# Performance work log

Measured on AMD Instinct MI355X. Metric: run time of the kernel, lower is better.

The kernel has to match this reference:

```python
import jax, jax.numpy as jnp
import numpy as np
from jax import lax

B, C, H, W = 32, 512, 14, 14
NA = 9
N = H * W * NA  # 1764 anchors per image
IOU_THR = 0.3
SCORE_THR = 0.5
TOPK = 50


def setup_inputs() -> dict:
    key = jax.random.key(0)
    ks = jax.random.split(key, 8)
    def w(k, shape):
        return jax.random.normal(k, shape, jnp.float32) * 0.01  # nn.init.normal_(std=0.01)
    inp = {"features": jax.random.normal(ks[0], (B, C, H, W), jnp.float32)}
    # bbox head: 512->256 (GN32) ->128 (GN16) ->128 (GN16) -> 4*NA (1x1)
    inp["b1w"] = w(ks[1], (256, 512, 3, 3)); inp["b1b"] = jnp.zeros(256)
    inp["bg1w"] = jnp.ones(256); inp["bg1b"] = jnp.zeros(256)
    inp["b2w"] = w(ks[2], (128, 256, 3, 3)); inp["b2b"] = jnp.zeros(128)
    inp["bg2w"] = jnp.ones(128); inp["bg2b"] = jnp.zeros(128)
    inp["b3w"] = w(ks[3], (128, 128, 3, 3)); inp["b3b"] = jnp.zeros(128)
    inp["bg3w"] = jnp.ones(128); inp["bg3b"] = jnp.zeros(128)
    inp["b4w"] = w(ks[4], (4 * NA, 128, 1, 1)); inp["b4b"] = jnp.zeros(4 * NA)
    # classification head: 512->256 (GN32) ->128 (GN16) -> NA (1x1)
    inp["c1w"] = w(ks[5], (256, 512, 3, 3)); inp["c1b"] = jnp.zeros(256)
    inp["cg1w"] = jnp.ones(256); inp["cg1b"] = jnp.zeros(256)
    inp["c2w"] = w(ks[6], (128, 256, 3, 3)); inp["c2b"] = jnp.zeros(128)
    inp["cg2w"] = jnp.ones(128); inp["cg2b"] = jnp.zeros(128)
    inp["c3w"] = w(ks[7], (NA, 128, 1, 1)); inp["c3b"] = jnp.zeros(NA)
    return inp


def conv(x, w, b):
    k = w.shape[-1]
    pad = ((k // 2, k // 2), (k // 2, k // 2))
    y = lax.conv_general_dilated(x, w, (1, 1), pad, dimension_numbers=("NCHW", "OIHW", "NCHW"))
    return y + b[None, :, None, None]


def group_norm(x, w, b, groups, eps=1e-5):
    Bn, Cn, Hn, Wn = x.shape
    xg = x.reshape(Bn, groups, Cn // groups, Hn, Wn)
    mu = xg.mean(axis=(2, 3, 4), keepdims=True)
    var = xg.var(axis=(2, 3, 4), keepdims=True)
    xg = (xg - mu) * lax.rsqrt(var + eps)
    return xg.reshape(Bn, Cn, Hn, Wn) * w[None, :, None, None] + b[None, :, None, None]


def gelu(x):
    return jax.nn.gelu(x, approximate=False)  # torch nn.GELU default (erf)


def nms_single(boxes, scores):
    # boxes [N,4], scores [N]; greedy NMS, fixed-shape padded output [TOPK,5]
    valid = scores > SCORE_THR
    boxes = jnp.clip(boxes, 0.0, 1.0)
    order = jnp.argsort(-jnp.where(valid, scores, -jnp.inf))  # desc, invalid last
    b = boxes[order]; s = scores[order]; v = valid[order]
    x1 = jnp.maximum(b[:, None, 0], b[None, :, 0])
    y1 = jnp.maximum(b[:, None, 1], b[None, :, 1])
    x2 = jnp.minimum(b[:, None, 2], b[None, :, 2])
    y2 = jnp.minimum(b[:, None, 3], b[None, :, 3])
    inter = jnp.clip(x2 - x1, 0.0) * jnp.clip(y2 - y1, 0.0)
    area = (b[:, 2] - b[:, 0]) * (b[:, 3] - b[:, 1])
    iou = inter / (area[:, None] + area[None, :] - inter)
    # torch keeps when iou < thr; NaN compares False -> suppressed. Replicate exactly:
    suppress = jnp.logical_not(iou < IOU_THR)  # [N,N] bool
    idxs = jnp.arange(N)
    def body(suppressed, xs):
        row, i, vi = xs
        keep_i = vi & jnp.logical_not(suppressed[i])
        return suppressed | (keep_i & row & (idxs > i)), keep_i
    _, keep = lax.scan(body, jnp.zeros(N, bool), (suppress, idxs, v))
    kept_scores = jnp.where(keep, s, -1.0)
    topv, topi = lax.top_k(kept_scores, TOPK)  # first <=50 kept in score order
    out_boxes = jnp.where(topv[:, None] > 0.0, b[topi], 0.0)
    return jnp.concatenate([out_boxes, topv[:, None]], axis=-1)  # [TOPK, 5]; score=-1 marks pad


def _forward(features, b1w, b1b, bg1w, bg1b, b2w, b2b, bg2w, bg2b, b3w, b3b, bg3w, bg3b, b4w, b4b, c1w, c1b, cg1w, cg1b, c2w, c2b, cg2w, cg2b, c3w, c3b):
    bs = features.shape[0]
    h = group_norm(gelu(conv(features, b1w, b1b)), bg1w, bg1b, 32)
    h = group_norm(gelu(conv(h, b2w, b2b)), bg2w, bg2b, 16)
    h = group_norm(gelu(conv(h, b3w, b3b)), bg3w, bg3b, 16)
    bbox = conv(h, b4w, b4b).transpose(0, 2, 3, 1).reshape(bs, -1, 4)  # [B,N,4]
    h = group_norm(gelu(conv(features, c1w, c1b)), cg1w, cg1b, 32)
    h = group_norm(gelu(conv(h, c2w, c2b)), cg2w, cg2b, 16)
    conf = jax.nn.sigmoid(conv(h, c3w, c3b).transpose(0, 2, 3, 1).reshape(bs, -1))  # [B,N]
    return jax.vmap(nms_single)(bbox, conf)  # [B,TOPK,5]


def reference(features, b1w, b1b, bg1w, bg1b, b2w, b2b, bg2w, bg2b, b3w, b3b, bg3w, bg3b, b4w, b4b, c1w, c1b, cg1w, cg1b, c2w, c2b, cg2w, cg2b, c3w, c3b):
    return _forward(features, b1w, b1b, bg1w, bg1b, b2w, b2b, bg2w, bg2b, b3w, b3b, bg3w, bg3b, b4w, b4b, c1w, c1b, cg1w, cg1b, c2w, c2b, cg2w, cg2b, c3w, c3b)
```

## Files before the change

### kernel.cpp

```cpp
#include <hip/hip_runtime.h>
#include <hip/hip_bf16.h>
#include <math.h>

#define CHUNK 16
#define NN 1764
#define SORTN 2048

typedef float v2f __attribute__((ext_vector_type(2)));

template<int Co, int Ci>
__device__ inline void seg_pack_pk(const float* __restrict__ src, float* __restrict__ dst, int i) {
  int co = i / (Ci * 9); int rem = i - co * (Ci * 9); int ci = rem / 9; int k = rem - ci * 9;
  int p = (co >> 5) * 16 + (co & 15);
  int h = (co & 31) >> 4;
  dst[((size_t)ci * (Co >> 1) + p) * 20 + 2 * k + h] = src[i];
}
template<int Co, int CiK>
__device__ inline void seg_tr(const float* __restrict__ src, float* __restrict__ dst, int i) {
  int co = i / CiK; int cik = i - co * CiK;
  dst[cik * Co + co] = src[i];
}

__global__ void wtrans_all(
  const float* __restrict__ b1w, const float* __restrict__ c1w,
  const float* __restrict__ b2w, const float* __restrict__ c2w,
  const float* __restrict__ b3w, const float* __restrict__ b4w,
  const float* __restrict__ c3w,
  float* __restrict__ wp1b, float* __restrict__ wp1c,
  float* __restrict__ wp2b, float* __restrict__ wp2c,
  float* __restrict__ wp3b, float* __restrict__ wt4b, float* __restrict__ wt3c)
{
  int j = blockIdx.x * blockDim.x + threadIdx.x;
  if (j < 1179648) { seg_pack_pk<256, 512>(b1w, wp1b, j); return; } j -= 1179648;
  if (j < 1179648) { seg_pack_pk<256, 512>(c1w, wp1c, j); return; } j -= 1179648;
  if (j < 294912)  { seg_pack_pk<128, 256>(b2w, wp2b, j); return; } j -= 294912;
  if (j < 294912)  { seg_pack_pk<128, 256>(c2w, wp2c, j); return; } j -= 294912;
  if (j < 147456)  { seg_pack_pk<128, 128>(b3w, wp3b, j); return; } j -= 147456;
  if (j < 4608)    { seg_tr<36, 128>(b4w, wt4b, j); return; }  j -= 4608;
  if (j < 1152)    { seg_tr<9, 128>(c3w, wt3c, j); return; }
}

template<int COPT>
__global__ __launch_bounds__(256, 2) void conv3x3_part(
    const float* __restrict__ in0, const float* __restrict__ in1,
    const float* __restrict__ wt0, const float* __restrict__ wt1,
    float* __restrict__ po0, float* __restrict__ po1,
    int Cin, int Cout, int cobPerHead, int cinPerSplit, size_t sStride)
{
  constexpr int NP = COPT / 2;
  const int tid = threadIdx.x;
  const int bx  = blockIdx.x;
  const int b   = blockIdx.y;
  const int s   = blockIdx.z;
  const int head = bx / cobPerHead;
  const int cob  = bx - head * cobPerHead;
  const float* in  = head ? in1  : in0;
  const float* wt  = head ? wt1  : wt0;
  float* po        = head ? po1  : po0;
  const int co0 = cob * (16 * COPT);

  const int col = tid & 15;
  const int r   = tid >> 4;
  const bool ract = r < 14;

  __shared__ float tile[2][CHUNK][16][16];

  {
    float* tz = &tile[0][0][0][0];
    for (int i = tid; i < 2 * CHUNK * 256; i += 256) tz[i] = 0.0f;
  }
  __syncthreads();

  const int p = tid;
  const bool pa = p < 196;
  const int prow = p / 14, pcol = p - prow * 14;
  const float* inb = in + (size_t)b * Cin * 196;
  const int cb0 = (s * cinPerSplit) / CHUNK;
  const int nch = cinPerSplit / CHUNK;
  const int CoutH = Cout >> 1;

  int pidx[NP];
#pragma unroll
  for (int g = 0; g < NP; ++g) pidx[g] = ((co0 >> 5) + g) * 16 + col;

  if (pa) {
#pragma unroll
    for (int ci = 0; ci < CHUNK; ++ci)
      tile[0][ci][prow + 1][pcol + 1] = inb[(cb0 * CHUNK + ci) * 196 + p];
  }
  __syncthreads();

  v2f acc[NP][14];
#pragma unroll
  for (int g = 0; g < NP; ++g)
#pragma unroll
    for (int j = 0; j < 14; ++j) acc[g][j] = (v2f)(0.0f);

  for (int lcb = 0; lcb < nch; ++lcb) {
    const int cbg = cb0 + lcb;
    const int cur = lcb & 1;
    const bool more = (lcb + 1 < nch);
    float v[CHUNK];
    if (more && pa) {
#pragma unroll
      for (int ci = 0; ci < CHUNK; ++ci)
        v[ci] = inb[((cbg + 1) * CHUNK + ci) * 196 + p];
    }
    if (ract) {
      for (int ci = 0; ci < CHUNK; ++ci) {
        v2f w2[NP][9];
#pragma unroll
        for (int g = 0; g < NP; ++g) {
          const float4* wq = (const float4*)(wt +
              ((size_t)(cbg * CHUNK + ci) * CoutH + pidx[g]) * 20);
          float4 q0 = wq[0], q1 = wq[1], q2 = wq[2], q3 = wq[3], q4 = wq[4];
          w2[g][0] = (v2f){q0.x, q0.y}; w2[g][1] = (v2f){q0.z, q0.w};
          w2[g][2] = (v2f){q1.x, q1.y}; w2[g][3] = (v2f){q1.z, q1.w};
          w2[g][4] = (v2f){q2.x, q2.y}; w2[g][5] = (v2f){q2.z, q2.w};
          w2[g][6] = (v2f){q3.x, q3.y}; w2[g][7] = (v2f){q3.z, q3.w};
          w2[g][8] = (v2f){q4.x, q4.y};
        }
        float nb[3][16];
#pragma unroll
        for (int dr = 0; dr < 3; ++dr) {
          const float4* rp = (const float4*)(&tile[cur][ci][r + dr][0]);
          float4 a = rp[0], bq = rp[1], cq = rp[2], dq = rp[3];
          nb[dr][0]  = a.x;  nb[dr][1]  = a.y;  nb[dr][2]  = a.z;  nb[dr][3]  = a.w;
          nb[dr][4]  = bq.x; nb[dr][5]  = bq.y; nb[dr][6]  = bq.z; nb[dr][7]  = bq.w;
          nb[dr][8]  = cq.x; nb[dr][9]  = cq.y; nb[dr][10] = cq.z; nb[dr][11] = cq.w;
          nb[dr][12] = dq.x; nb[dr][13] = dq.y; nb[dr][14] = dq.z; nb[dr][15] = dq.w;
        }
#pragma unroll
        for (int ky = 0; ky < 3; ++ky)
#pragma unroll
          for (int kx = 0; kx < 3; ++kx) {
#pragma unroll
            for (int g = 0; g < NP; ++g) {
              v2f w = w2[g][ky * 3 + kx];
#pragma unroll
              for (int j = 0; j < 14; ++j) {
                float s_ = nb[ky][j + kx];
                v2f nbv = (v2f){s_, s_};
                acc[g][j] = __builtin_elementwise_fma(w, nbv, acc[g][j]);
              }
            }
          }
      }
    }
    if (more && pa) {
#pragma unroll
      for (int ci = 0; ci < CHUNK; ++ci)
        tile[1 - cur][ci][prow + 1][pcol + 1] = v[ci];
    }
    __syncthreads();
  }

  if (ract) {
#pragma unroll
    for (int g = 0; g < NP; ++g) {
      const int ocx = 32 * g + col;
      const int ocy = ocx + 16;
      float* opx = po + (size_t)s * sStride + ((size_t)b * Cout + co0 + ocx) * 196 + r * 14;
      float* opy = po + (size_t)s * sStride + ((size_t)b * Cout + co0 + ocy) * 196 + r * 14;
#pragma unroll
      for (int j = 0; j < 14; ++j) { opx[j] = acc[g][j].x; opy[j] = acc[g][j].y; }
    }
  }
}

template<int S>
__global__ __launch_bounds__(256) void combine_gn(
    const float* __restrict__ po0, const float* __restrict__ po1,
    const float* __restrict__ bs0, const float* __restrict__ bs1,
    const float* __restrict__ gw0, const float* __restrict__ gw1,
    const float* __restrict__ gb0, const float* __restrict__ gb1,
    float* __restrict__ out0, float* __restrict__ out1,
    int Cout, int cobPerHead, size_t sStride)
{
  const int tid = threadIdx.x, bx = blockIdx.x, b = blockIdx.y;
  const int head = bx / cobPerHead, cob = bx - head * cobPerHead;
  const float* po = head ? po1 : po0;
  const float* bs = head ? bs1 : bs0;
  const float* gw = head ? gw1 : gw0;
  const float* gb = head ? gb1 : gb0;
  float* out      = head ? out1 : out0;
  const int co0 = cob * 16;

  __shared__ float red[4][4];
  __shared__ float stats[4];

  const int p = tid;
  const bool pa = p < 196;
  float v[16];
  float s0 = 0.f, q0 = 0.f, s1 = 0.f, q1 = 0.f;
  if (pa) {
#pragma unroll
    for (int c = 0; c < 16; ++c) {
      const size_t base = ((size_t)b * Cout + co0 + c) * 196 + p;
      float x = bs[co0 + c];
#pragma unroll
      for (int s = 0; s < S; ++s) x += po[base + (size_t)s * sStride];
      float g = 0.5f * x * (1.0f + erff(x * 0.70710678118654752440f));
      v[c] = g;
      if (c < 8) { s0 += g; q0 += g * g; } else { s1 += g; q1 += g * g; }
    }
  }
#pragma unroll
  for (int off = 32; off > 0; off >>= 1) {
    s0 += __shfl_down(s0, off, 64); q0 += __shfl_down(q0, off, 64);
    s1 += __shfl_down(s1, off, 64); q1 += __shfl_down(q1, off, 64);
  }
  const int wave = tid >> 6, lane = tid & 63;
  if (lane == 0) { red[wave][0] = s0; red[wave][1] = q0; red[wave][2] = s1; red[wave][3] = q1; }
  __syncthreads();
  if (tid == 0) {
    float S0 = red[0][0] + red[1][0] + red[2][0] + red[3][0];
    float Q0 = red[0][1] + red[1][1] + red[2][1] + red[3][1];
    float S1 = red[0][2] + red[1][2] + red[2][2] + red[3][2];
    float Q1 = red[0][3] + red[1][3] + red[2][3] + red[3][3];
    float m0 = S0 * (1.0f / 1568.0f);
    float v0 = Q0 * (1.0f / 1568.0f) - m0 * m0;
    float m1 = S1 * (1.0f / 1568.0f);
    float v1 = Q1 * (1.0f / 1568.0f) - m1 * m1;
    stats[0] = m0; stats[1] = 1.0f / sqrtf(v0 + 1e-5f);
    stats[2] = m1; stats[3] = 1.0f / sqrtf(v1 + 1e-5f);
  }
  __syncthreads();
  if (pa) {
    float m0 = stats[0], i0 = stats[1], m1 = stats[2], i1 = stats[3];
#pragma unroll
    for (int c = 0; c < 16; ++c) {
      float m  = (c < 8) ? m0 : m1;
      float iv = (c < 8) ? i0 : i1;
      float y = (v[c] - m) * iv * gw[co0 + c] + gb[co0 + c];
      out[((size_t)b * Cout + co0 + c) * 196 + p] = y;
    }
  }
}

__global__ __launch_bounds__(256) void heads_1x1(
    const float* __restrict__ tb, const float* __restrict__ tc,
    const float* __restrict__ wtb, const float* __restrict__ wtc,
    const float* __restrict__ bb,  const float* __restrict__ bc,
    float* __restrict__ bbox, float* __restrict__ conf)
{
  const int b = blockIdx.x, og = blockIdx.y, tid = threadIdx.x;
  if (tid >= 196) return;
  const int p = tid;
  const bool isConf = (og == 4);
  const float* in = isConf ? tc : tb;
  const float* wbase = isConf ? wtc : (wtb + og * 9);
  const int wstride = isConf ? 9 : 36;
  const float* bsrc = isConf ? bc : (bb + og * 9);

  float a[9];
#pragma unroll
  for (int o = 0; o < 9; ++o) a[o] = bsrc[o];
  const float* pin = in + (size_t)b * 128 * 196 + p;
  for (int ci = 0; ci < 128; ++ci) {
    float x = pin[ci * 196];
    const float* w = wbase + ci * wstride;
#pragma unroll
    for (int o = 0; o < 9; ++o) a[o] = fmaf(w[o], x, a[o]);
  }
  if (isConf) {
    float* cf = conf + (size_t)b * NN + (size_t)p * 9;
#pragma unroll
    for (int o = 0; o < 9; ++o) cf[o] = 1.0f / (1.0f + expf(-a[o]));
  } else {
    float* bp = bbox + ((size_t)b * NN) * 4 + (size_t)p * 36 + og * 9;
#pragma unroll
    for (int o = 0; o < 9; ++o) bp[o] = a[o];
  }
}

__global__ __launch_bounds__(512) void nms_kernel(
  const float* __restrict__ bbox, const float* __restrict__ conf, float* __restrict__ out)
{
  const int b = blockIdx.x, tid = threadIdx.x;
  __shared__ unsigned long long key[SORTN];
  __shared__ float sx1[NN], sy1[NN], sx2[NN], sy2[NN], sar[NN], ssc[NN];
  __shared__ unsigned char sup[NN];
  __shared__ int sV, sMin;

  if (tid == 0) sV = 0;
  __syncthreads();
  int cntv = 0;
  const float* cf = conf + (size_t)b * NN;
  for (int i = tid; i < SORTN; i += 512) {
    unsigned long long k;
    if (i < NN) {
      float s = cf[i];
      unsigned rank = (unsigned)(NN - 1 - i);
      if (s > 0.5f) { k = (((unsigned long long)__float_as_uint(s)) << 32) | rank; cntv++; }
      else k = (unsigned long long)rank;
    } else k = 0ull;
    key[i] = k;
  }
  atomicAdd(&sV, cntv);
  __syncthreads();
  const int V = sV;

  for (int kk = 2; kk <= SORTN; kk <<= 1) {
    for (int j = kk >> 1; j > 0; j >>= 1) {
      for (int i = tid; i < SORTN; i += 512) {
        int ixj = i ^ j;
        if (ixj > i) {
          unsigned long long a = key[i], c = key[ixj];
          bool dirDesc = ((i & kk) == 0);
          if ((a < c) == dirDesc) { key[i] = c; key[ixj] = a; }
        }
      }
      __syncthreads();
    }
  }

  const float* bbb = bbox + (size_t)b * NN * 4;
  for (int i = tid; i < V; i += 512) {
    unsigned long long k = key[i];
    int idx = NN - 1 - (int)(unsigned)(k & 0xFFFFFFFFull);
    float s = __uint_as_float((unsigned)(k >> 32));
    const float* bp = bbb + (size_t)idx * 4;
    float x1 = fminf(fmaxf(bp[0], 0.0f), 1.0f);
    float y1 = fminf(fmaxf(bp[1], 0.0f), 1.0f);
    float x2 = fminf(fmaxf(bp[2], 0.0f), 1.0f);
    float y2 = fminf(fmaxf(bp[3], 0.0f), 1.0f);
    sx1[i] = x1; sy1[i] = y1; sx2[i] = x2; sy2[i] = y2;
    sar[i] = (x2 - x1) * (y2 - y1);
    ssc[i] = s;
    sup[i] = 0;
  }
  __syncthreads();

  int kept = 0, cur = 0;
  float* ob = out + (size_t)b * 50 * 5;
  while (kept < 50 && cur < V) {
    int nxt = -1;
    for (int base = cur; base < V; base += 512) {
      if (tid == 0) sMin = 0x7FFFFFFF;
      __syncthreads();
      int i = base + tid;
      if (i < V && !sup[i]) atomicMin(&sMin, i);
      __syncthreads();
      if (sMin != 0x7FFFFFFF) { nxt = sMin; break; }
    }
    if (nxt < 0) break;
    float kx1 = sx1[nxt], ky1 = sy1[nxt], kx2 = sx2[nxt], ky2 = sy2[nxt], ka = sar[nxt];
    if (tid == 0) {
      float* rr = ob + kept * 5;
      rr[0] = kx1; rr[1] = ky1; rr[2] = kx2; rr[3] = ky2; rr[4] = ssc[nxt];
    }
    kept++;
    for (int jj = nxt + 1 + tid; jj < V; jj += 512) {
      if (!sup[jj]) {
        float xx1 = fmaxf(kx1, sx1[jj]);
        float yy1 = fmaxf(ky1, sy1[jj]);
        float xx2 = fminf(kx2, sx2[jj]);
        float yy2 = fminf(ky2, sy2[jj]);
        float inter = fmaxf(xx2 - xx1, 0.0f) * fmaxf(yy2 - yy1, 0.0f);
        float iou = inter / ((ka + sar[jj]) - inter);
        if (!(iou < 0.3f)) sup[jj] = 1;
      }
    }
    cur = nxt + 1;
    __syncthreads();
  }
  for (int rr = kept + tid; rr < 50; rr += 512) {
    float* qq = ob + rr * 5;
    qq[0] = 0.0f; qq[1] = 0.0f; qq[2] = 0.0f; qq[3] = 0.0f; qq[4] = -1.0f;
  }
}

extern "C" void kernel_launch(void* const* d_in, const int* in_sizes, int n_in,
                              void* d_out, int out_size, void* d_ws, size_t ws_size,
                              hipStream_t stream)
{
  const float* features = (const float*)d_in[0];
  const float* b1w = (const float*)d_in[1];  const float* b1b = (const float*)d_in[2];
  const float* bg1w = (const float*)d_in[3]; const float* bg1b = (const float*)d_in[4];
  const float* b2w = (const float*)d_in[5];  const float* b2b = (const float*)d_in[6];
  const float* bg2w = (const float*)d_in[7]; const float* bg2b = (const float*)d_in[8];
  const float* b3w = (const float*)d_in[9];  const float* b3b = (const float*)d_in[10];
  const float* bg3w = (const float*)d_in[11]; const float* bg3b = (const float*)d_in[12];
  const float* b4w = (const float*)d_in[13]; const float* b4b = (const float*)d_in[14];
  const float* c1w = (const float*)d_in[15]; const float* c1b = (const float*)d_in[16];
  const float* cg1w = (const float*)d_in[17]; const float* cg1b = (const float*)d_in[18];
  const float* c2w = (const float*)d_in[19]; const float* c2b = (const float*)d_in[20];
  const float* cg2w = (const float*)d_in[21]; const float* cg2b = (const float*)d_in[22];
  const float* c3w = (const float*)d_in[23]; const float* c3b = (const float*)d_in[24];

  float* ws = (float*)d_ws;
  float* wp1b = ws; ws += 1310720;
  float* wp1c = ws; ws += 1310720;
  float* wp2b = ws; ws += 327680;
  float* wp2c = ws; ws += 327680;
  float* wp3b = ws; ws += 163840;
  float* wt4b = ws; ws += 4608;
  float* wt3c = ws; ws += 1152;
  float* t1b = ws; ws += 1605632;
  float* t1c = ws; ws += 1605632;
  float* t2b = ws; ws += 802816;
  float* t2c = ws; ws += 802816;
  float* P   = ws; ws += 12845056;
  float* bbox = ws; ws += 225792;
  float* conf = ws; ws += 56448;
  float* t3b = t1b;

  wtrans_all<<<12119, 256, 0, stream>>>(b1w, c1w, b2w, c2w, b3w, b4w, c3w,
                                        wp1b, wp1c, wp2b, wp2c, wp3b, wt4b, wt3c);

  {
    const size_t sStr = (size_t)32 * 256 * 196;
    conv3x3_part<4><<<dim3(8, 32, 4), 256, 0, stream>>>(
        features, features, wp1b, wp1c, P, P + 4 * sStr, 512, 256, 4, 128, sStr);
    combine_gn<4><<<dim3(32, 32), 256, 0, stream>>>(
        P, P + 4 * sStr, b1b, c1b, bg1w, cg1w, bg1b, cg1b, t1b, t1c, 256, 16, sStr);
  }
  {
    const size_t sStr = (size_t)32 * 128 * 196;
    conv3x3_part<4><<<dim3(4, 32, 8), 256, 0, stream>>>(
        t1b, t1c, wp2b, wp2c, P, P + 8 * sStr, 256, 128, 2, 32, sStr);
    combine_gn<8><<<dim3(16, 32), 256, 0, stream>>>(
        P, P + 8 * sStr, b2b, c2b, bg2w, cg2w, bg2b, cg2b, t2b, t2c, 128, 8, sStr);
  }
  {
    const size_t sStr = (size_t)32 * 128 * 196;
    conv3x3_part<2><<<dim3(4, 32, 8), 256, 0, stream>>>(
        t2b, t2b, wp3b, wp3b, P, P, 128, 128, 4, 16, sStr);
    combine_gn<8><<<dim3(8, 32), 256, 0, stream>>>(
        P, P, b3b, b3b, bg3w, bg3w, bg3b, bg3b, t3b, t3b, 128, 8, sStr);
  }

  heads_1x1<<<dim3(32, 5), 256, 0, stream>>>(t3b, t2c, wt4b, wt3c, b4b, c3b, bbox, conf);
  nms_kernel<<<32, 512, 0, stream>>>(bbox, conf, (float*)d_out);
}
```

Baseline: 777.0 us.

## Store activations in padded 16x16 layout and load conv tiles via LDS DMA

Activations are now stored in a zero-padded 16x16-per-channel layout, written directly by combine_gn and by a new pad_in kernel for the input features. This lets the conv kernels stream each input chunk into shared memory with global_load_lds DMA instead of register staging and scattered LDS stores. The aim is to cut register pressure and LDS store work in the conv inner loop. NMS also compacts only valid scores, sorts a smaller power-of-two array, and uses 1024 threads. The cost is an extra padding pass over the features and about 30% more activation memory traffic.

```diff
diff --git a/kernel.cpp b/kernel.cpp
--- a/kernel.cpp
+++ b/kernel.cpp
@@ -7,6 +7,12 @@
 #define SORTN 2048
 
 typedef float v2f __attribute__((ext_vector_type(2)));
+
+__device__ inline void lds_dma16(const float* g, float* l) {
+  __builtin_amdgcn_global_load_lds(
+      (const __attribute__((address_space(1))) void*)g,
+      (__attribute__((address_space(3))) void*)l, 16, 0, 0);
+}
 
 template<int Co, int Ci>
 __device__ inline void seg_pack_pk(const float* __restrict__ src, float* __restrict__ dst, int i) {
@@ -38,6 +44,18 @@
   if (j < 147456)  { seg_pack_pk<128, 128>(b3w, wp3b, j); return; } j -= 147456;
   if (j < 4608)    { seg_tr<36, 128>(b4w, wt4b, j); return; }  j -= 4608;
   if (j < 1152)    { seg_tr<9, 128>(c3w, wt3c, j); return; }
+}
+
+__global__ __launch_bounds__(256) void pad_in(const float* __restrict__ in,
+                                              float* __restrict__ out)
+{
+  int idx = blockIdx.x * 256 + threadIdx.x;
+  int cell = idx & 255, ch = idx >> 8;
+  int ly = cell >> 4, lx = cell & 15;
+  bool inter = (ly >= 1) && (ly <= 14) && (lx >= 1) && (lx <= 14);
+  float v = 0.0f;
+  if (inter) v = in[ch * 196 + (ly - 1) * 14 + (lx - 1)];
+  out[idx] = v;
 }
 
 template<int COPT>
@@ -62,19 +80,11 @@
   const int col = tid & 15;
   const int r   = tid >> 4;
   const bool ract = r < 14;
-
-  __shared__ float tile[2][CHUNK][16][16];
-
-  {
-    float* tz = &tile[0][0][0][0];
-    for (int i = tid; i < 2 * CHUNK * 256; i += 256) tz[i] = 0.0f;
-  }
-  __syncthreads();
-
-  const int p = tid;
-  const bool pa = p < 196;
-  const int prow = p / 14, pcol = p - prow * 14;
-  const float* inb = in + (size_t)b * Cin * 196;
+  const int wv = tid >> 6, lane = tid & 63;
+
+  __shared__ float tile[2][CHUNK][256];
+
+  const float* inb = in + ((size_t)b * Cin + (size_t)s * cinPerSplit) * 256;
   const int cb0 = (s * cinPerSplit) / CHUNK;
   const int nch = cinPerSplit / CHUNK;
   const int CoutH = Cout >> 1;
@@ -83,10 +93,10 @@
 #pragma unroll
   for (int g = 0; g < NP; ++g) pidx[g] = ((co0 >> 5) + g) * 16 + col;
 
-  if (pa) {
-#pragma unroll
-    for (int ci = 0; ci < CHUNK; ++ci)
-      tile[0][ci][prow + 1][pcol + 1] = inb[(cb0 * CHUNK + ci) * 196 + p];
+#pragma unroll
+  for (int k = 0; k < 4; ++k) {
+    int ci = wv * 4 + k;
+    lds_dma16(inb + ci * 256 + lane * 4, &tile[0][ci][0]);
   }
   __syncthreads();
 
@@ -99,12 +109,13 @@
   for (int lcb = 0; lcb < nch; ++lcb) {
     const int cbg = cb0 + lcb;
     const int cur = lcb & 1;
-    const bool more = (lcb + 1 < nch);
-    float v[CHUNK];
-    if (more && pa) {
-#pragma unroll
-      for (int ci = 0; ci < CHUNK; ++ci)
-        v[ci] = inb[((cbg + 1) * CHUNK + ci) * 196 + p];
+    if (lcb + 1 < nch) {
+      const float* nx = inb + (size_t)(lcb + 1) * CHUNK * 256;
+#pragma unroll
+      for (int k = 0; k < 4; ++k) {
+        int ci = wv * 4 + k;
+        lds_dma16(nx + ci * 256 + lane * 4, &tile[1 - cur][ci][0]);
+      }
     }
     if (ract) {
       for (int ci = 0; ci < CHUNK; ++ci) {
@@ -123,7 +134,7 @@
         float nb[3][16];
 #pragma unroll
         for (int dr = 0; dr < 3; ++dr) {
-          const float4* rp = (const float4*)(&tile[cur][ci][r + dr][0]);
+          const float4* rp = (const float4*)(&tile[cur][ci][(r + dr) * 16]);
           float4 a = rp[0], bq = rp[1], cq = rp[2], dq = rp[3];
           nb[dr][0]  = a.x;  nb[dr][1]  = a.y;  nb[dr][2]  = a.z;  nb[dr][3]  = a.w;
           nb[dr][4]  = bq.x; nb[dr][5]  = bq.y; nb[dr][6]  = bq.z; nb[dr][7]  = bq.w;
@@ -147,11 +158,6 @@
           }
       }
     }
-    if (more && pa) {
-#pragma unroll
-      for (int ci = 0; ci < CHUNK; ++ci)
-        tile[1 - cur][ci][prow + 1][pcol + 1] = v[ci];
-    }
     __syncthreads();
   }
 
@@ -189,11 +195,13 @@
   __shared__ float red[4][4];
   __shared__ float stats[4];
 
-  const int p = tid;
-  const bool pa = p < 196;
+  const int ly = tid >> 4, lx = tid & 15;
+  const bool inter = (ly >= 1) && (ly <= 14) && (lx >= 1) && (lx <= 14);
+  const int p = (ly - 1) * 14 + (lx - 1);
+
   float v[16];
   float s0 = 0.f, q0 = 0.f, s1 = 0.f, q1 = 0.f;
-  if (pa) {
+  if (inter) {
 #pragma unroll
     for (int c = 0; c < 16; ++c) {
       const size_t base = ((size_t)b * Cout + co0 + c) * 196 + p;
@@ -226,15 +234,16 @@
     stats[2] = m1; stats[3] = 1.0f / sqrtf(v1 + 1e-5f);
   }
   __syncthreads();
-  if (pa) {
-    float m0 = stats[0], i0 = stats[1], m1 = stats[2], i1 = stats[3];
-#pragma unroll
-    for (int c = 0; c < 16; ++c) {
+  float m0 = stats[0], i0 = stats[1], m1 = stats[2], i1 = stats[3];
+#pragma unroll
+  for (int c = 0; c < 16; ++c) {
+    float y = 0.0f;
+    if (inter) {
       float m  = (c < 8) ? m0 : m1;
       float iv = (c < 8) ? i0 : i1;
-      float y = (v[c] - m) * iv * gw[co0 + c] + gb[co0 + c];
-      out[((size_t)b * Cout + co0 + c) * 196 + p] = y;
-    }
+      y = (v[c] - m) * iv * gw[co0 + c] + gb[co0 + c];
+    }
+    out[((size_t)b * Cout + co0 + c) * 256 + tid] = y;
   }
 }
 
@@ -247,6 +256,8 @@
   const int b = blockIdx.x, og = blockIdx.y, tid = threadIdx.x;
   if (tid >= 196) return;
   const int p = tid;
+  const int prow = p / 14, pcol = p - prow * 14;
+  const int pp = (prow + 1) * 16 + (pcol + 1);
   const bool isConf = (og == 4);
   const float* in = isConf ? tc : tb;
   const float* wbase = isConf ? wtc : (wtb + og * 9);
@@ -256,9 +267,9 @@
   float a[9];
 #pragma unroll
   for (int o = 0; o < 9; ++o) a[o] = bsrc[o];
-  const float* pin = in + (size_t)b * 128 * 196 + p;
+  const float* pin = in + (size_t)b * 128 * 256 + pp;
   for (int ci = 0; ci < 128; ++ci) {
-    float x = pin[ci * 196];
+    float x = pin[ci * 256];
     const float* w = wbase + ci * wstride;
 #pragma unroll
     for (int o = 0; o < 9; ++o) a[o] = fmaf(w[o], x, a[o]);
@@ -274,7 +285,7 @@
   }
 }
 
-__global__ __launch_bounds__(512) void nms_kernel(
+__global__ __launch_bounds__(1024) void nms_kernel(
   const float* __restrict__ bbox, const float* __restrict__ conf, float* __restrict__ out)
 {
   const int b = blockIdx.x, tid = threadIdx.x;
@@ -285,25 +296,24 @@
 
   if (tid == 0) sV = 0;
   __syncthreads();
-  int cntv = 0;
   const float* cf = conf + (size_t)b * NN;
-  for (int i = tid; i < SORTN; i += 512) {
-    unsigned long long k;
-    if (i < NN) {
-      float s = cf[i];
-      unsigned rank = (unsigned)(NN - 1 - i);
-      if (s > 0.5f) { k = (((unsigned long long)__float_as_uint(s)) << 32) | rank; cntv++; }
-      else k = (unsigned long long)rank;
-    } else k = 0ull;
-    key[i] = k;
-  }
-  atomicAdd(&sV, cntv);
+  for (int i = tid; i < NN; i += 1024) {
+    float s = cf[i];
+    if (s > 0.5f) {
+      int slot = atomicAdd(&sV, 1);
+      key[slot] = (((unsigned long long)__float_as_uint(s)) << 32)
+                | (unsigned)(NN - 1 - i);
+    }
+  }
   __syncthreads();
   const int V = sV;
-
-  for (int kk = 2; kk <= SORTN; kk <<= 1) {
+  const int SN = (V <= 1024) ? 1024 : 2048;
+  for (int i = V + tid; i < SN; i += 1024) key[i] = 0ull;
+  __syncthreads();
+
+  for (int kk = 2; kk <= SN; kk <<= 1) {
     for (int j = kk >> 1; j > 0; j >>= 1) {
-      for (int i = tid; i < SORTN; i += 512) {
+      for (int i = tid; i < SN; i += 1024) {
         int ixj = i ^ j;
         if (ixj > i) {
           unsigned long long a = key[i], c = key[ixj];
@@ -316,7 +326,7 @@
   }
 
   const float* bbb = bbox + (size_t)b * NN * 4;
-  for (int i = tid; i < V; i += 512) {
+  for (int i = tid; i < V; i += 1024) {
     unsigned long long k = key[i];
     int idx = NN - 1 - (int)(unsigned)(k & 0xFFFFFFFFull);
     float s = __uint_as_float((unsigned)(k >> 32));
@@ -336,7 +346,7 @@
   float* ob = out + (size_t)b * 50 * 5;
   while (kept < 50 && cur < V) {
     int nxt = -1;
-    for (int base = cur; base < V; base += 512) {
+    for (int base = cur; base < V; base += 1024) {
       if (tid == 0) sMin = 0x7FFFFFFF;
       __syncthreads();
       int i = base + tid;
@@ -351,7 +361,7 @@
       rr[0] = kx1; rr[1] = ky1; rr[2] = kx2; rr[3] = ky2; rr[4] = ssc[nxt];
     }
     kept++;
-    for (int jj = nxt + 1 + tid; jj < V; jj += 512) {
+    for (int jj = nxt + 1 + tid; jj < V; jj += 1024) {
       if (!sup[jj]) {
         float xx1 = fmaxf(kx1, sx1[jj]);
         float yy1 = fmaxf(ky1, sy1[jj]);
@@ -365,7 +375,7 @@
     cur = nxt + 1;
     __syncthreads();
   }
-  for (int rr = kept + tid; rr < 50; rr += 512) {
+  for (int rr = kept + tid; rr < 50; rr += 1024) {
     float* qq = ob + rr * 5;
     qq[0] = 0.0f; qq[1] = 0.0f; qq[2] = 0.0f; qq[3] = 0.0f; qq[4] = -1.0f;
   }
@@ -397,10 +407,11 @@
   float* wp3b = ws; ws += 163840;
   float* wt4b = ws; ws += 4608;
   float* wt3c = ws; ws += 1152;
-  float* t1b = ws; ws += 1605632;
-  float* t1c = ws; ws += 1605632;
-  float* t2b = ws; ws += 802816;
-  float* t2c = ws; ws += 802816;
+  float* fpad = ws; ws += 4194304;
+  float* t1b = ws; ws += 2097152;
+  float* t1c = ws; ws += 2097152;
+  float* t2b = ws; ws += 1048576;
+  float* t2c = ws; ws += 1048576;
   float* P   = ws; ws += 12845056;
   float* bbox = ws; ws += 225792;
   float* conf = ws; ws += 56448;
@@ -408,11 +419,12 @@
 
   wtrans_all<<<12119, 256, 0, stream>>>(b1w, c1w, b2w, c2w, b3w, b4w, c3w,
                                         wp1b, wp1c, wp2b, wp2c, wp3b, wt4b, wt3c);
+  pad_in<<<16384, 256, 0, stream>>>(features, fpad);
 
   {
     const size_t sStr = (size_t)32 * 256 * 196;
     conv3x3_part<4><<<dim3(8, 32, 4), 256, 0, stream>>>(
-        features, features, wp1b, wp1c, P, P + 4 * sStr, 512, 256, 4, 128, sStr);
+        fpad, fpad, wp1b, wp1c, P, P + 4 * sStr, 512, 256, 4, 128, sStr);
     combine_gn<4><<<dim3(32, 32), 256, 0, stream>>>(
         P, P + 4 * sStr, b1b, c1b, bg1w, cg1w, bg1b, cg1b, t1b, t1c, 256, 16, sStr);
   }
@@ -432,5 +444,5 @@
   }
 
   heads_1x1<<<dim3(32, 5), 256, 0, stream>>>(t3b, t2c, wt4b, wt3c, b4b, c3b, bbox, conf);
-  nms_kernel<<<32, 512, 0, stream>>>(bbox, conf, (float*)d_out);
-}
+  nms_kernel<<<32, 1024, 0, stream>>>(bbox, conf, (float*)d_out);
+}
```

Result: slower. 870.4 us (+12.0%).
